# Kernel optimization log

Hardware: AMD Instinct MI355X
Metric: run time of the kernel (lower is better)

## Reference

```python
import jax, jax.numpy as jnp
import numpy as np

B, V, NV, NR, N, E, D, H, OUT, L = 4, 20, 8000, 200, 8000, 200000, 128, 128, 64, 3
DECAY = 0.03


def setup_inputs() -> dict:
    key = jax.random.key(0)
    ks = jax.random.split(key, 16)
    node_ids = jax.random.randint(ks[0], (N,), 0, NV)
    rel_ids = jax.random.randint(ks[1], (E,), 0, NR)
    edge_index = jax.random.randint(ks[2], (2, E), 0, N)
    batch = jnp.repeat(jnp.arange(B), N // B)  # sorted graph assignment, 2000 nodes/graph
    visit_node = (jax.random.uniform(ks[3], (B, V, NV)) < 0.3).astype(jnp.float32)
    ehr_nodes = (jax.random.uniform(ks[4], (B, NV)) < 0.1).astype(jnp.float32)
    s = lambda k, shape: jax.random.normal(k, shape, jnp.float32) * 0.05
    return dict(
        node_ids=node_ids, rel_ids=rel_ids, edge_index=edge_index, batch=batch,
        visit_node=visit_node, ehr_nodes=ehr_nodes,
        node_emb_w=s(ks[5], (NV, D)), rel_emb_w=s(ks[6], (NR, D)),
        lin_w=s(ks[7], (D, H)), lin_b=jnp.zeros((H,), jnp.float32),
        alpha_w=s(ks[8], (L, H)), alpha_b=jnp.zeros((L,), jnp.float32),
        beta_w=s(ks[9], (L, NV)), beta_b=jnp.zeros((L,), jnp.float32),
        conv_w=s(ks[10], (L, H, H)), conv_b=jnp.zeros((L, H), jnp.float32),
        wr_w=s(ks[11], (L, H)), wr_b=jnp.zeros((L,), jnp.float32),
        mlp_w=s(ks[12], (2 * H, OUT)), mlp_b=jnp.zeros((OUT,), jnp.float32),
    )


def reference(node_ids, rel_ids, edge_index, batch, visit_node, ehr_nodes,
              node_emb_w, rel_emb_w, lin_w, lin_b, alpha_w, alpha_b,
              beta_w, beta_b, conv_w, conv_b, wr_w, wr_b, mlp_w, mlp_b):
    # shared input projection (torch: self.lin applied to node and edge embeddings)
    x = node_emb_w[node_ids] @ lin_w + lin_b          # [N,H]
    edge_attr = rel_emb_w[rel_ids] @ lin_w + lin_b    # [E,H]

    # pack per-graph node features into dense [B, NV, H] (x_new in torch, fixed across layers)
    counts = jax.ops.segment_sum(jnp.ones((N,), jnp.float32), batch, B)            # [B]
    starts = jnp.concatenate([jnp.zeros((1,), jnp.int32),
                              jnp.cumsum(counts.astype(jnp.int32))[:-1]])
    local = jnp.arange(N) - starts[batch]                                          # position within graph
    x_pad = jnp.zeros((B, NV, H), jnp.float32).at[batch, local].set(x)

    lam = jnp.exp(DECAY * (V - jnp.arange(V, dtype=jnp.float32)))[None, :, None]   # [1,V,1]
    src, dst = edge_index[0], edge_index[1]
    eb, en = batch[src], node_ids[src]

    for l in range(L):
        # alpha attention over visits (softmax on visit axis)
        feat = visit_node[..., None] * x_pad[:, None]                              # [B,V,NV,H]
        alpha = jax.nn.softmax(jnp.einsum('bvnh,h->bvn', feat, alpha_w[l]) + alpha_b[l], axis=1)
        # beta: time-decayed visit attention
        beta = jnp.tanh(visit_node @ beta_w[l] + beta_b[l])[:, :, None] * lam      # [B,V,1]
        attn_full = alpha * beta                                                   # [B,V,NV]
        attn_e = attn_full[eb, 0, en][:, None]                                     # [E,1] (visit idx 0 as in source)
        # BiAttentionGNNConv: gather-mul-relu-scatter with edge attention
        w_rel = (edge_attr @ wr_w[l] + wr_b[l])[:, None]                           # [E,1]
        msg = jax.nn.relu(x[src] * attn_e + w_rel * edge_attr)                     # [E,H]
        agg = jax.ops.segment_sum(msg, dst, N)                                     # scatter-add to targets
        x = jax.nn.relu((agg + x) @ conv_w[l] + conv_b[l])                         # eps=0 -> (1+eps)*x = x; dropout=eval

    # joint patient representation
    x_graph = jax.ops.segment_sum(x, batch, B) / counts[:, None]                   # global mean pool
    x_node = (ehr_nodes @ node_emb_w) / jnp.sum(ehr_nodes, axis=1, keepdims=True)  # [B,D]
    x_node = x_node @ lin_w + lin_b
    logits = jnp.concatenate([x_graph, x_node], axis=1) @ mlp_w + mlp_b            # [B,OUT]
    return logits
```

## Files before the change

kernel.cpp:

```cpp
#include <hip/hip_runtime.h>

#define NN  8000
#define EE  200000
#define BB  4
#define VV  20
#define NVV 8000
#define NRR 200
#define HH  128
#define OO  64
#define LL  3
#define NPB 8

__global__ void k_zero(float* fz, int nf, int* iz, int ni) {
  int i = blockIdx.x * 256 + threadIdx.x;
  if (i < nf) fz[i] = 0.f;
  if (i < ni) iz[i] = 0;
}

__global__ __launch_bounds__(128) void k_proj_nodes(
    const int* __restrict__ node_ids, const float* __restrict__ emb,
    const float* __restrict__ lin_w, const float* __restrict__ lin_b,
    const float* __restrict__ alpha_w, float* __restrict__ x,
    float* __restrict__ snode)
{
  int blk = blockIdx.x, t = threadIdx.x;
  __shared__ float er[NPB][HH];
  __shared__ float part[LL][NPB][2];
  int base = blk * NPB;
  #pragma unroll
  for (int n = 0; n < NPB; ++n)
    er[n][t] = emb[node_ids[base + n] * HH + t];
  __syncthreads();
  float bt = lin_b[t];
  float acc[NPB];
  #pragma unroll
  for (int n = 0; n < NPB; ++n) acc[n] = bt;
  for (int d4 = 0; d4 < HH / 4; ++d4) {
    float e4[NPB][4];
    #pragma unroll
    for (int n = 0; n < NPB; ++n) {
      float4 v = *(const float4*)&er[n][d4 * 4];
      e4[n][0] = v.x; e4[n][1] = v.y; e4[n][2] = v.z; e4[n][3] = v.w;
    }
    #pragma unroll
    for (int j = 0; j < 4; ++j) {
      float lwv = lin_w[(d4 * 4 + j) * HH + t];
      #pragma unroll
      for (int n = 0; n < NPB; ++n) acc[n] += e4[n][j] * lwv;
    }
  }
  #pragma unroll
  for (int n = 0; n < NPB; ++n) x[(base + n) * HH + t] = acc[n];
  #pragma unroll
  for (int l = 0; l < LL; ++l) {
    float aw = alpha_w[l * HH + t];
    #pragma unroll
    for (int n = 0; n < NPB; ++n) {
      float v = acc[n] * aw;
      for (int off = 32; off > 0; off >>= 1) v += __shfl_down(v, off, 64);
      if ((t & 63) == 0) part[l][n][t >> 6] = v;
    }
  }
  __syncthreads();
  if (t < LL * NPB) {
    int l = t / NPB, n = t % NPB;
    snode[l * NN + base + n] = part[l][n][0] + part[l][n][1];
  }
}

__global__ __launch_bounds__(128) void k_proj_rels(
    const float* __restrict__ rel_emb, const float* __restrict__ lin_w,
    const float* __restrict__ lin_b, const float* __restrict__ wr_w,
    const float* __restrict__ wr_b, float* __restrict__ wrelp)
{
  int r = blockIdx.x, t = threadIdx.x;
  __shared__ float row[HH];
  __shared__ float part[LL][2];
  row[t] = rel_emb[r * HH + t];
  __syncthreads();
  float acc = lin_b[t];
  #pragma unroll 4
  for (int d = 0; d < HH; ++d) acc += row[d] * lin_w[d * HH + t];
  #pragma unroll
  for (int l = 0; l < LL; ++l) {
    float v = acc * wr_w[l * HH + t];
    for (int off = 32; off > 0; off >>= 1) v += __shfl_down(v, off, 64);
    if ((t & 63) == 0) part[l][t >> 6] = v;
  }
  __syncthreads();
  #pragma unroll
  for (int l = 0; l < LL; ++l) {
    float rd = part[l][0] + part[l][1] + wr_b[l];
    wrelp[(l * NRR + r) * HH + t] = rd * acc;
  }
}

__global__ __launch_bounds__(256) void k_beta(
    const float* __restrict__ visit_node, const float* __restrict__ beta_w,
    const float* __restrict__ beta_b, float* __restrict__ beta0)
{
  int l = blockIdx.x >> 2, b = blockIdx.x & 3, t = threadIdx.x;
  __shared__ float red[256];
  float acc = 0.f;
  for (int n = t; n < NVV; n += 256)
    acc += visit_node[(b * VV + 0) * NVV + n] * beta_w[l * NVV + n];
  red[t] = acc;
  __syncthreads();
  for (int s = 128; s > 0; s >>= 1) {
    if (t < s) red[t] += red[t + s];
    __syncthreads();
  }
  if (t == 0) beta0[l * BB + b] = tanhf(red[0] + beta_b[l]) * expf(0.03f * 20.0f);
}

__global__ __launch_bounds__(256) void k_attn(
    const float* __restrict__ visit_node, const float* __restrict__ snode,
    const float* __restrict__ alpha_b, float* __restrict__ attn0)
{
  int idx = blockIdx.x * 256 + threadIdx.x;
  if (idx >= BB * NVV) return;
  int b = idx / NVV, n = idx % NVV;
  float vn[VV];
  #pragma unroll
  for (int v = 0; v < VV; ++v) vn[v] = visit_node[(b * VV + v) * NVV + n];
  for (int l = 0; l < LL; ++l) {
    float s = (n < NN / BB) ? snode[l * NN + b * (NN / BB) + n] : 0.0f;
    float ab = alpha_b[l];
    float m = -1e30f;
    #pragma unroll
    for (int v = 0; v < VV; ++v) m = fmaxf(m, vn[v] * s + ab);
    float sum = 0.f;
    #pragma unroll
    for (int v = 0; v < VV; ++v) sum += expf(vn[v] * s + ab - m);
    attn0[(l * BB + b) * NVV + n] = expf(vn[0] * s + ab - m) / sum;
  }
}

__global__ void k_anode(const int* __restrict__ node_ids, const int* __restrict__ batch,
                        const float* __restrict__ attn0, const float* __restrict__ beta0,
                        float* __restrict__ anode)
{
  int i = blockIdx.x * 256 + threadIdx.x;
  if (i >= NN) return;
  int b = batch[i], nid = node_ids[i];
  #pragma unroll
  for (int l = 0; l < LL; ++l)
    anode[l * NN + i] = attn0[(l * BB + b) * NVV + nid] * beta0[l * BB + b];
}

__global__ void k_hist(const int* __restrict__ edge_index, int* __restrict__ deg) {
  int e = blockIdx.x * 256 + threadIdx.x;
  if (e >= EE) return;
  atomicAdd(&deg[edge_index[EE + e]], 1);
}

__global__ __launch_bounds__(1024) void k_scan(const int* __restrict__ deg,
                                               int* __restrict__ row_ptr)
{
  int t = threadIdx.x;
  __shared__ int ps[1024];
  int local[8];
  int base = t * 8;
  int s = 0;
  #pragma unroll
  for (int j = 0; j < 8; ++j) {
    int idx = base + j;
    int v = (idx < NN) ? deg[idx] : 0;
    local[j] = s; s += v;
  }
  ps[t] = s;
  __syncthreads();
  for (int off = 1; off < 1024; off <<= 1) {
    int v = (t >= off) ? ps[t - off] : 0;
    __syncthreads();
    ps[t] += v;
    __syncthreads();
  }
  int excl = (t == 0) ? 0 : ps[t - 1];
  #pragma unroll
  for (int j = 0; j < 8; ++j) {
    int idx = base + j;
    if (idx < NN) row_ptr[idx] = excl + local[j];
  }
  if (t == 1023) row_ptr[NN] = ps[1023];
}

__global__ void k_scatter(const int* __restrict__ edge_index, const int* __restrict__ rel_ids,
                          const int* __restrict__ row_ptr, int* __restrict__ cursor,
                          int2* __restrict__ csr_sr, float* __restrict__ csr_a,
                          const float* __restrict__ anode)
{
  int e = blockIdx.x * 256 + threadIdx.x;
  if (e >= EE) return;
  int src = edge_index[e];
  int dst = edge_index[EE + e];
  int rid = rel_ids[e];
  int p = row_ptr[dst] + atomicAdd(&cursor[dst], 1);
  csr_sr[p] = make_int2(src, rid);
  csr_a[0 * EE + p] = anode[0 * NN + src];
  csr_a[1 * EE + p] = anode[1 * NN + src];
  csr_a[2 * EE + p] = anode[2 * NN + src];
}

__global__ __launch_bounds__(256) void k_gather_conv(
    const int* __restrict__ row_ptr, const int2* __restrict__ csr_sr,
    const float* __restrict__ csr_a, const float* __restrict__ xin,
    const float* __restrict__ wrelp, const float* __restrict__ conv_w,
    const float* __restrict__ conv_b, float* __restrict__ xout, int l)
{
  int t = threadIdx.x;
  int sub = t >> 5, lane = t & 31;
  int i = blockIdx.x * NPB + sub;
  __shared__ float aggrow[NPB][HH];
  const float4* __restrict__ xin4 = (const float4*)xin;
  const float4* __restrict__ wr4 = (const float4*)wrelp + (size_t)l * NRR * 32;
  const float4* __restrict__ cw4 = (const float4*)conv_w + (size_t)l * HH * 32;
  const float* __restrict__ ca = csr_a + (size_t)l * EE;

  float4 acc = xin4[i * 32 + lane];
  int k0 = row_ptr[i], k1 = row_ptr[i + 1];
  int k = k0;
  for (; k + 1 < k1; k += 2) {
    int2 sr0 = csr_sr[k];
    int2 sr1 = csr_sr[k + 1];
    float a0 = ca[k], a1 = ca[k + 1];
    float4 x0 = xin4[sr0.x * 32 + lane];
    float4 w0 = wr4[sr0.y * 32 + lane];
    float4 x1 = xin4[sr1.x * 32 + lane];
    float4 w1 = wr4[sr1.y * 32 + lane];
    acc.x += fmaxf(x0.x * a0 + w0.x, 0.f) + fmaxf(x1.x * a1 + w1.x, 0.f);
    acc.y += fmaxf(x0.y * a0 + w0.y, 0.f) + fmaxf(x1.y * a1 + w1.y, 0.f);
    acc.z += fmaxf(x0.z * a0 + w0.z, 0.f) + fmaxf(x1.z * a1 + w1.z, 0.f);
    acc.w += fmaxf(x0.w * a0 + w0.w, 0.f) + fmaxf(x1.w * a1 + w1.w, 0.f);
  }
  if (k < k1) {
    int2 sr0 = csr_sr[k];
    float a0 = ca[k];
    float4 x0 = xin4[sr0.x * 32 + lane];
    float4 w0 = wr4[sr0.y * 32 + lane];
    acc.x += fmaxf(x0.x * a0 + w0.x, 0.f);
    acc.y += fmaxf(x0.y * a0 + w0.y, 0.f);
    acc.z += fmaxf(x0.z * a0 + w0.z, 0.f);
    acc.w += fmaxf(x0.w * a0 + w0.w, 0.f);
  }
  *(float4*)&aggrow[sub][lane * 4] = acc;
  __syncthreads();

  float4 o = ((const float4*)conv_b)[l * 32 + lane];
  for (int d4 = 0; d4 < HH / 4; ++d4) {
    float4 ag = *(const float4*)&aggrow[sub][d4 * 4];
    float4 c0 = cw4[(d4 * 4 + 0) * 32 + lane];
    float4 c1 = cw4[(d4 * 4 + 1) * 32 + lane];
    float4 c2 = cw4[(d4 * 4 + 2) * 32 + lane];
    float4 c3 = cw4[(d4 * 4 + 3) * 32 + lane];
    o.x += ag.x * c0.x + ag.y * c1.x + ag.z * c2.x + ag.w * c3.x;
    o.y += ag.x * c0.y + ag.y * c1.y + ag.z * c2.y + ag.w * c3.y;
    o.z += ag.x * c0.z + ag.y * c1.z + ag.z * c2.z + ag.w * c3.z;
    o.w += ag.x * c0.w + ag.y * c1.w + ag.z * c2.w + ag.w * c3.w;
  }
  o.x = fmaxf(o.x, 0.f); o.y = fmaxf(o.y, 0.f);
  o.z = fmaxf(o.z, 0.f); o.w = fmaxf(o.w, 0.f);
  ((float4*)xout)[i * 32 + lane] = o;
}

__global__ __launch_bounds__(128) void k_xgraph(
    const float* __restrict__ x, float* __restrict__ xg_raw)
{
  int b = blockIdx.x >> 4, c = blockIdx.x & 15, t = threadIdx.x;
  const int per = (NN / BB) / 16;
  int base = b * (NN / BB) + c * per;
  float acc = 0.f;
  for (int i = 0; i < per; ++i) acc += x[(base + i) * HH + t];
  atomicAdd(&xg_raw[b * HH + t], acc);
}

__global__ __launch_bounds__(128) void k_xnode(
    const float* __restrict__ ehr, const float* __restrict__ emb,
    float* __restrict__ xn_raw, float* __restrict__ denom)
{
  int b = blockIdx.x >> 5, c = blockIdx.x & 31, t = threadIdx.x;
  const int per = NVV / 32;
  int base = c * per;
  float acc = 0.f;
  for (int n = base; n < base + per; ++n)
    acc += ehr[b * NVV + n] * emb[n * HH + t];
  atomicAdd(&xn_raw[b * HH + t], acc);
  __shared__ float red[128];
  float dsum = 0.f;
  for (int n = base + t; n < base + per; n += 128) dsum += ehr[b * NVV + n];
  red[t] = dsum;
  __syncthreads();
  for (int s = 64; s > 0; s >>= 1) {
    if (t < s) red[t] += red[t + s];
    __syncthreads();
  }
  if (t == 0) atomicAdd(&denom[b], red[0]);
}

__global__ __launch_bounds__(128) void k_final(
    const float* __restrict__ xg_raw, const float* __restrict__ xn_raw,
    const float* __restrict__ denom, const float* __restrict__ lin_w,
    const float* __restrict__ lin_b, const float* __restrict__ mlp_w,
    const float* __restrict__ mlp_b, float* __restrict__ out)
{
  int b = blockIdx.x, t = threadIdx.x;
  __shared__ float xg[HH], xn[HH], xnp[HH];
  xg[t] = xg_raw[b * HH + t] * (1.0f / (NN / BB));
  xn[t] = xn_raw[b * HH + t] / denom[b];
  __syncthreads();
  float a3 = lin_b[t];
  #pragma unroll 4
  for (int d = 0; d < HH; ++d) a3 += xn[d] * lin_w[d * HH + t];
  xnp[t] = a3;
  __syncthreads();
  if (t < OO) {
    float a4 = mlp_b[t];
    #pragma unroll 4
    for (int h = 0; h < HH; ++h)
      a4 += xg[h] * mlp_w[h * OO + t] + xnp[h] * mlp_w[(HH + h) * OO + t];
    out[b * OO + t] = a4;
  }
}

extern "C" void kernel_launch(void* const* d_in, const int* in_sizes, int n_in,
                              void* d_out, int out_size, void* d_ws, size_t ws_size,
                              hipStream_t stream) {
  const int*   node_ids   = (const int*)d_in[0];
  const int*   rel_ids    = (const int*)d_in[1];
  const int*   edge_index = (const int*)d_in[2];
  const int*   batch      = (const int*)d_in[3];
  const float* visit_node = (const float*)d_in[4];
  const float* ehr        = (const float*)d_in[5];
  const float* node_emb   = (const float*)d_in[6];
  const float* rel_emb    = (const float*)d_in[7];
  const float* lin_w      = (const float*)d_in[8];
  const float* lin_b      = (const float*)d_in[9];
  const float* alpha_w    = (const float*)d_in[10];
  const float* alpha_b    = (const float*)d_in[11];
  const float* beta_w     = (const float*)d_in[12];
  const float* beta_b     = (const float*)d_in[13];
  const float* conv_w     = (const float*)d_in[14];
  const float* conv_b     = (const float*)d_in[15];
  const float* wr_w       = (const float*)d_in[16];
  const float* wr_b       = (const float*)d_in[17];
  const float* mlp_w      = (const float*)d_in[18];
  const float* mlp_b      = (const float*)d_in[19];
  float* out = (float*)d_out;

  float* ws = (float*)d_ws;
  float* xA     = ws; ws += NN * HH;
  float* xB     = ws; ws += NN * HH;
  float* wrelp  = ws; ws += LL * NRR * HH;
  float* snode  = ws; ws += LL * NN;
  float* beta0  = ws; ws += LL * BB;
  float* attn0  = ws; ws += LL * BB * NVV;
  float* anode  = ws; ws += LL * NN;
  float* xg_raw = ws; ws += BB * HH;
  float* xn_raw = ws; ws += BB * HH;
  float* denom  = ws; ws += BB;
  int* iws      = (int*)ws;
  int* deg      = iws; iws += NN;
  int* cursor   = iws; iws += NN;
  int* row_ptr  = iws; iws += NN + 2;
  int2* csr_sr  = (int2*)iws; iws += 2 * EE;
  float* csr_a  = (float*)iws;

  int nf = BB * HH * 2 + BB;
  int ni = 2 * NN;
  hipLaunchKernelGGL(k_zero, dim3((ni + 255) / 256), dim3(256), 0, stream,
                     xg_raw, nf, deg, ni);

  hipLaunchKernelGGL(k_proj_nodes, dim3(NN / NPB), dim3(HH), 0, stream,
                     node_ids, node_emb, lin_w, lin_b, alpha_w, xA, snode);
  hipLaunchKernelGGL(k_proj_rels, dim3(NRR), dim3(HH), 0, stream,
                     rel_emb, lin_w, lin_b, wr_w, wr_b, wrelp);
  hipLaunchKernelGGL(k_beta, dim3(LL * BB), dim3(256), 0, stream,
                     visit_node, beta_w, beta_b, beta0);
  hipLaunchKernelGGL(k_attn, dim3((BB * NVV + 255) / 256), dim3(256), 0, stream,
                     visit_node, snode, alpha_b, attn0);
  hipLaunchKernelGGL(k_anode, dim3((NN + 255) / 256), dim3(256), 0, stream,
                     node_ids, batch, attn0, beta0, anode);

  hipLaunchKernelGGL(k_hist, dim3((EE + 255) / 256), dim3(256), 0, stream,
                     edge_index, deg);
  hipLaunchKernelGGL(k_scan, dim3(1), dim3(1024), 0, stream, deg, row_ptr);
  hipLaunchKernelGGL(k_scatter, dim3((EE + 255) / 256), dim3(256), 0, stream,
                     edge_index, rel_ids, row_ptr, cursor, csr_sr, csr_a, anode);

  const float* xin = xA;
  float* xout = xB;
  for (int l = 0; l < LL; ++l) {
    hipLaunchKernelGGL(k_gather_conv, dim3(NN / NPB), dim3(256), 0, stream,
                       row_ptr, csr_sr, csr_a, xin, wrelp, conv_w, conv_b, xout, l);
    const float* tmp = xin; xin = xout; xout = (float*)tmp;
  }

  hipLaunchKernelGGL(k_xgraph, dim3(BB * 16), dim3(HH), 0, stream, xB, xg_raw);
  hipLaunchKernelGGL(k_xnode, dim3(BB * 32), dim3(HH), 0, stream,
                     ehr, node_emb, xn_raw, denom);
  hipLaunchKernelGGL(k_final, dim3(BB), dim3(HH), 0, stream,
                     xg_raw, xn_raw, denom, lin_w, lin_b, mlp_w, mlp_b, out);
}
```

Measured before the change: 320.7 us.

## Fuse small setup kernels and gather per-node attention directly in conv

Merges the zeroing, relation projection and beta reduction into one kernel. Attention is computed only for the nodes actually used, fused with the degree histogram. The two pooling kernels become one. The scatter no longer writes per-edge attention arrays; the gather kernel reads anode[src] directly and is unrolled by 4. This cuts launch count, the full attn0 table computation and per-edge attention writes, at the cost of an extra indirect load per edge in each conv layer.

```diff
diff --git a/kernel.cpp b/kernel.cpp
--- a/kernel.cpp
+++ b/kernel.cpp
@@ -10,12 +10,7 @@
 #define OO  64
 #define LL  3
 #define NPB 8
-
-__global__ void k_zero(float* fz, int nf, int* iz, int ni) {
-  int i = blockIdx.x * 256 + threadIdx.x;
-  if (i < nf) fz[i] = 0.f;
-  if (i < ni) iz[i] = 0;
-}
+#define NG  2000
 
 __global__ __launch_bounds__(128) void k_proj_nodes(
     const int* __restrict__ node_ids, const float* __restrict__ emb,
@@ -68,63 +63,70 @@
   }
 }
 
-__global__ __launch_bounds__(128) void k_proj_rels(
+__global__ __launch_bounds__(128) void k_prb(
     const float* __restrict__ rel_emb, const float* __restrict__ lin_w,
     const float* __restrict__ lin_b, const float* __restrict__ wr_w,
-    const float* __restrict__ wr_b, float* __restrict__ wrelp)
-{
-  int r = blockIdx.x, t = threadIdx.x;
-  __shared__ float row[HH];
-  __shared__ float part[LL][2];
-  row[t] = rel_emb[r * HH + t];
-  __syncthreads();
-  float acc = lin_b[t];
-  #pragma unroll 4
-  for (int d = 0; d < HH; ++d) acc += row[d] * lin_w[d * HH + t];
+    const float* __restrict__ wr_b, const float* __restrict__ visit_node,
+    const float* __restrict__ beta_w, const float* __restrict__ beta_b,
+    float* __restrict__ wrelp, float* __restrict__ beta0,
+    int* __restrict__ iz, float* __restrict__ fz)
+{
+  int blk = blockIdx.x, t = threadIdx.x;
+  int idx = blk * 128 + t;
+  if (idx < 2 * NN) iz[idx] = 0;
+  if (idx < BB * HH * 2 + BB) fz[idx] = 0.f;
+  if (blk < NRR) {
+    __shared__ float row[HH];
+    __shared__ float part[LL][2];
+    row[t] = rel_emb[blk * HH + t];
+    __syncthreads();
+    float acc = lin_b[t];
+    #pragma unroll 4
+    for (int d = 0; d < HH; ++d) acc += row[d] * lin_w[d * HH + t];
+    #pragma unroll
+    for (int l = 0; l < LL; ++l) {
+      float v = acc * wr_w[l * HH + t];
+      for (int off = 32; off > 0; off >>= 1) v += __shfl_down(v, off, 64);
+      if ((t & 63) == 0) part[l][t >> 6] = v;
+    }
+    __syncthreads();
+    #pragma unroll
+    for (int l = 0; l < LL; ++l) {
+      float rd = part[l][0] + part[l][1] + wr_b[l];
+      wrelp[(l * NRR + blk) * HH + t] = rd * acc;
+    }
+  } else {
+    int j = blk - NRR;
+    int l = j >> 2, b = j & 3;
+    float acc = 0.f;
+    for (int n = t; n < NVV; n += 128)
+      acc += visit_node[(b * VV + 0) * NVV + n] * beta_w[l * NVV + n];
+    for (int off = 32; off > 0; off >>= 1) acc += __shfl_down(acc, off, 64);
+    __shared__ float bred[2];
+    if ((t & 63) == 0) bred[t >> 6] = acc;
+    __syncthreads();
+    if (t == 0)
+      beta0[l * BB + b] = tanhf(bred[0] + bred[1] + beta_b[l]) * expf(0.03f * 20.0f);
+  }
+}
+
+__global__ __launch_bounds__(256) void k_anode_hist(
+    const int* __restrict__ node_ids, const int* __restrict__ batch,
+    const int* __restrict__ edge_index, const float* __restrict__ visit_node,
+    const float* __restrict__ snode, const float* __restrict__ alpha_b,
+    const float* __restrict__ beta0, float* __restrict__ anode,
+    int* __restrict__ deg)
+{
+  int idx = blockIdx.x * 256 + threadIdx.x;
+  if (idx < EE) atomicAdd(&deg[edge_index[EE + idx]], 1);
+  if (idx >= NN) return;
+  int b = batch[idx], nid = node_ids[idx];
+  float vn[VV];
+  #pragma unroll
+  for (int v = 0; v < VV; ++v) vn[v] = visit_node[(b * VV + v) * NVV + nid];
   #pragma unroll
   for (int l = 0; l < LL; ++l) {
-    float v = acc * wr_w[l * HH + t];
-    for (int off = 32; off > 0; off >>= 1) v += __shfl_down(v, off, 64);
-    if ((t & 63) == 0) part[l][t >> 6] = v;
-  }
-  __syncthreads();
-  #pragma unroll
-  for (int l = 0; l < LL; ++l) {
-    float rd = part[l][0] + part[l][1] + wr_b[l];
-    wrelp[(l * NRR + r) * HH + t] = rd * acc;
-  }
-}
-
-__global__ __launch_bounds__(256) void k_beta(
-    const float* __restrict__ visit_node, const float* __restrict__ beta_w,
-    const float* __restrict__ beta_b, float* __restrict__ beta0)
-{
-  int l = blockIdx.x >> 2, b = blockIdx.x & 3, t = threadIdx.x;
-  __shared__ float red[256];
-  float acc = 0.f;
-  for (int n = t; n < NVV; n += 256)
-    acc += visit_node[(b * VV + 0) * NVV + n] * beta_w[l * NVV + n];
-  red[t] = acc;
-  __syncthreads();
-  for (int s = 128; s > 0; s >>= 1) {
-    if (t < s) red[t] += red[t + s];
-    __syncthreads();
-  }
-  if (t == 0) beta0[l * BB + b] = tanhf(red[0] + beta_b[l]) * expf(0.03f * 20.0f);
-}
-
-__global__ __launch_bounds__(256) void k_attn(
-    const float* __restrict__ visit_node, const float* __restrict__ snode,
-    const float* __restrict__ alpha_b, float* __restrict__ attn0)
-{
-  int idx = blockIdx.x * 256 + threadIdx.x;
-  if (idx >= BB * NVV) return;
-  int b = idx / NVV, n = idx % NVV;
-  float vn[VV];
-  #pragma unroll
-  for (int v = 0; v < VV; ++v) vn[v] = visit_node[(b * VV + v) * NVV + n];
-  for (int l = 0; l < LL; ++l) {
-    float s = (n < NN / BB) ? snode[l * NN + b * (NN / BB) + n] : 0.0f;
+    float s = (nid < NG) ? snode[l * NN + b * NG + nid] : 0.0f;
     float ab = alpha_b[l];
     float m = -1e30f;
     #pragma unroll
@@ -132,26 +134,8 @@
     float sum = 0.f;
     #pragma unroll
     for (int v = 0; v < VV; ++v) sum += expf(vn[v] * s + ab - m);
-    attn0[(l * BB + b) * NVV + n] = expf(vn[0] * s + ab - m) / sum;
-  }
-}
-
-__global__ void k_anode(const int* __restrict__ node_ids, const int* __restrict__ batch,
-                        const float* __restrict__ attn0, const float* __restrict__ beta0,
-                        float* __restrict__ anode)
-{
-  int i = blockIdx.x * 256 + threadIdx.x;
-  if (i >= NN) return;
-  int b = batch[i], nid = node_ids[i];
-  #pragma unroll
-  for (int l = 0; l < LL; ++l)
-    anode[l * NN + i] = attn0[(l * BB + b) * NVV + nid] * beta0[l * BB + b];
-}
-
-__global__ void k_hist(const int* __restrict__ edge_index, int* __restrict__ deg) {
-  int e = blockIdx.x * 256 + threadIdx.x;
-  if (e >= EE) return;
-  atomicAdd(&deg[edge_index[EE + e]], 1);
+    anode[l * NN + idx] = (expf(vn[0] * s + ab - m) / sum) * beta0[l * BB + b];
+  }
 }
 
 __global__ __launch_bounds__(1024) void k_scan(const int* __restrict__ deg,
@@ -187,24 +171,18 @@
 
 __global__ void k_scatter(const int* __restrict__ edge_index, const int* __restrict__ rel_ids,
                           const int* __restrict__ row_ptr, int* __restrict__ cursor,
-                          int2* __restrict__ csr_sr, float* __restrict__ csr_a,
-                          const float* __restrict__ anode)
+                          int2* __restrict__ csr_sr)
 {
   int e = blockIdx.x * 256 + threadIdx.x;
   if (e >= EE) return;
-  int src = edge_index[e];
   int dst = edge_index[EE + e];
-  int rid = rel_ids[e];
   int p = row_ptr[dst] + atomicAdd(&cursor[dst], 1);
-  csr_sr[p] = make_int2(src, rid);
-  csr_a[0 * EE + p] = anode[0 * NN + src];
-  csr_a[1 * EE + p] = anode[1 * NN + src];
-  csr_a[2 * EE + p] = anode[2 * NN + src];
+  csr_sr[p] = make_int2(edge_index[e], rel_ids[e]);
 }
 
 __global__ __launch_bounds__(256) void k_gather_conv(
     const int* __restrict__ row_ptr, const int2* __restrict__ csr_sr,
-    const float* __restrict__ csr_a, const float* __restrict__ xin,
+    const float* __restrict__ anode, const float* __restrict__ xin,
     const float* __restrict__ wrelp, const float* __restrict__ conv_w,
     const float* __restrict__ conv_b, float* __restrict__ xout, int l)
 {
@@ -215,29 +193,32 @@
   const float4* __restrict__ xin4 = (const float4*)xin;
   const float4* __restrict__ wr4 = (const float4*)wrelp + (size_t)l * NRR * 32;
   const float4* __restrict__ cw4 = (const float4*)conv_w + (size_t)l * HH * 32;
-  const float* __restrict__ ca = csr_a + (size_t)l * EE;
+  const float* __restrict__ an = anode + (size_t)l * NN;
 
   float4 acc = xin4[i * 32 + lane];
   int k0 = row_ptr[i], k1 = row_ptr[i + 1];
   int k = k0;
-  for (; k + 1 < k1; k += 2) {
-    int2 sr0 = csr_sr[k];
-    int2 sr1 = csr_sr[k + 1];
-    float a0 = ca[k], a1 = ca[k + 1];
-    float4 x0 = xin4[sr0.x * 32 + lane];
-    float4 w0 = wr4[sr0.y * 32 + lane];
-    float4 x1 = xin4[sr1.x * 32 + lane];
-    float4 w1 = wr4[sr1.y * 32 + lane];
-    acc.x += fmaxf(x0.x * a0 + w0.x, 0.f) + fmaxf(x1.x * a1 + w1.x, 0.f);
-    acc.y += fmaxf(x0.y * a0 + w0.y, 0.f) + fmaxf(x1.y * a1 + w1.y, 0.f);
-    acc.z += fmaxf(x0.z * a0 + w0.z, 0.f) + fmaxf(x1.z * a1 + w1.z, 0.f);
-    acc.w += fmaxf(x0.w * a0 + w0.w, 0.f) + fmaxf(x1.w * a1 + w1.w, 0.f);
-  }
-  if (k < k1) {
-    int2 sr0 = csr_sr[k];
-    float a0 = ca[k];
-    float4 x0 = xin4[sr0.x * 32 + lane];
-    float4 w0 = wr4[sr0.y * 32 + lane];
+  for (; k + 3 < k1; k += 4) {
+    int2 s0 = csr_sr[k],     s1 = csr_sr[k + 1];
+    int2 s2 = csr_sr[k + 2], s3 = csr_sr[k + 3];
+    float a0 = an[s0.x], a1 = an[s1.x], a2 = an[s2.x], a3 = an[s3.x];
+    float4 x0 = xin4[s0.x * 32 + lane], w0 = wr4[s0.y * 32 + lane];
+    float4 x1 = xin4[s1.x * 32 + lane], w1 = wr4[s1.y * 32 + lane];
+    float4 x2 = xin4[s2.x * 32 + lane], w2 = wr4[s2.y * 32 + lane];
+    float4 x3 = xin4[s3.x * 32 + lane], w3 = wr4[s3.y * 32 + lane];
+    acc.x += fmaxf(x0.x * a0 + w0.x, 0.f) + fmaxf(x1.x * a1 + w1.x, 0.f)
+           + fmaxf(x2.x * a2 + w2.x, 0.f) + fmaxf(x3.x * a3 + w3.x, 0.f);
+    acc.y += fmaxf(x0.y * a0 + w0.y, 0.f) + fmaxf(x1.y * a1 + w1.y, 0.f)
+           + fmaxf(x2.y * a2 + w2.y, 0.f) + fmaxf(x3.y * a3 + w3.y, 0.f);
+    acc.z += fmaxf(x0.z * a0 + w0.z, 0.f) + fmaxf(x1.z * a1 + w1.z, 0.f)
+           + fmaxf(x2.z * a2 + w2.z, 0.f) + fmaxf(x3.z * a3 + w3.z, 0.f);
+    acc.w += fmaxf(x0.w * a0 + w0.w, 0.f) + fmaxf(x1.w * a1 + w1.w, 0.f)
+           + fmaxf(x2.w * a2 + w2.w, 0.f) + fmaxf(x3.w * a3 + w3.w, 0.f);
+  }
+  for (; k < k1; ++k) {
+    int2 s0 = csr_sr[k];
+    float a0 = an[s0.x];
+    float4 x0 = xin4[s0.x * 32 + lane], w0 = wr4[s0.y * 32 + lane];
     acc.x += fmaxf(x0.x * a0 + w0.x, 0.f);
     acc.y += fmaxf(x0.y * a0 + w0.y, 0.f);
     acc.z += fmaxf(x0.z * a0 + w0.z, 0.f);
@@ -263,38 +244,39 @@
   ((float4*)xout)[i * 32 + lane] = o;
 }
 
-__global__ __launch_bounds__(128) void k_xgraph(
-    const float* __restrict__ x, float* __restrict__ xg_raw)
-{
-  int b = blockIdx.x >> 4, c = blockIdx.x & 15, t = threadIdx.x;
-  const int per = (NN / BB) / 16;
-  int base = b * (NN / BB) + c * per;
-  float acc = 0.f;
-  for (int i = 0; i < per; ++i) acc += x[(base + i) * HH + t];
-  atomicAdd(&xg_raw[b * HH + t], acc);
-}
-
-__global__ __launch_bounds__(128) void k_xnode(
-    const float* __restrict__ ehr, const float* __restrict__ emb,
+__global__ __launch_bounds__(128) void k_pool(
+    const float* __restrict__ x, const float* __restrict__ ehr,
+    const float* __restrict__ emb, float* __restrict__ xg_raw,
     float* __restrict__ xn_raw, float* __restrict__ denom)
 {
-  int b = blockIdx.x >> 5, c = blockIdx.x & 31, t = threadIdx.x;
-  const int per = NVV / 32;
-  int base = c * per;
-  float acc = 0.f;
-  for (int n = base; n < base + per; ++n)
-    acc += ehr[b * NVV + n] * emb[n * HH + t];
-  atomicAdd(&xn_raw[b * HH + t], acc);
-  __shared__ float red[128];
-  float dsum = 0.f;
-  for (int n = base + t; n < base + per; n += 128) dsum += ehr[b * NVV + n];
-  red[t] = dsum;
-  __syncthreads();
-  for (int s = 64; s > 0; s >>= 1) {
-    if (t < s) red[t] += red[t + s];
-    __syncthreads();
-  }
-  if (t == 0) atomicAdd(&denom[b], red[0]);
+  int t = threadIdx.x;
+  if (blockIdx.x < 64) {
+    int b = blockIdx.x >> 4, c = blockIdx.x & 15;
+    const int per = NG / 16;
+    int base = b * NG + c * per;
+    float acc = 0.f;
+    for (int i = 0; i < per; ++i) acc += x[(base + i) * HH + t];
+    atomicAdd(&xg_raw[b * HH + t], acc);
+  } else {
+    int ib = blockIdx.x - 64;
+    int b = ib >> 5, c = ib & 31;
+    const int per = NVV / 32;
+    int base = c * per;
+    float acc = 0.f;
+    for (int n = base; n < base + per; ++n)
+      acc += ehr[b * NVV + n] * emb[n * HH + t];
+    atomicAdd(&xn_raw[b * HH + t], acc);
+    __shared__ float red[128];
+    float dsum = 0.f;
+    for (int n = base + t; n < base + per; n += 128) dsum += ehr[b * NVV + n];
+    red[t] = dsum;
+    __syncthreads();
+    for (int s = 64; s > 0; s >>= 1) {
+      if (t < s) red[t] += red[t + s];
+      __syncthreads();
+    }
+    if (t == 0) atomicAdd(&denom[b], red[0]);
+  }
 }
 
 __global__ __launch_bounds__(128) void k_final(
@@ -305,7 +287,7 @@
 {
   int b = blockIdx.x, t = threadIdx.x;
   __shared__ float xg[HH], xn[HH], xnp[HH];
-  xg[t] = xg_raw[b * HH + t] * (1.0f / (NN / BB));
+  xg[t] = xg_raw[b * HH + t] * (1.0f / NG);
   xn[t] = xn_raw[b * HH + t] / denom[b];
   __syncthreads();
   float a3 = lin_b[t];
@@ -353,7 +335,6 @@
   float* wrelp  = ws; ws += LL * NRR * HH;
   float* snode  = ws; ws += LL * NN;
   float* beta0  = ws; ws += LL * BB;
-  float* attn0  = ws; ws += LL * BB * NVV;
   float* anode  = ws; ws += LL * NN;
   float* xg_raw = ws; ws += BB * HH;
   float* xn_raw = ws; ws += BB * HH;
@@ -362,42 +343,28 @@
   int* deg      = iws; iws += NN;
   int* cursor   = iws; iws += NN;
   int* row_ptr  = iws; iws += NN + 2;
-  int2* csr_sr  = (int2*)iws; iws += 2 * EE;
-  float* csr_a  = (float*)iws;
-
-  int nf = BB * HH * 2 + BB;
-  int ni = 2 * NN;
-  hipLaunchKernelGGL(k_zero, dim3((ni + 255) / 256), dim3(256), 0, stream,
-                     xg_raw, nf, deg, ni);
+  int2* csr_sr  = (int2*)iws;
 
   hipLaunchKernelGGL(k_proj_nodes, dim3(NN / NPB), dim3(HH), 0, stream,
                      node_ids, node_emb, lin_w, lin_b, alpha_w, xA, snode);
-  hipLaunchKernelGGL(k_proj_rels, dim3(NRR), dim3(HH), 0, stream,
-                     rel_emb, lin_w, lin_b, wr_w, wr_b, wrelp);
-  hipLaunchKernelGGL(k_beta, dim3(LL * BB), dim3(256), 0, stream,
-                     visit_node, beta_w, beta_b, beta0);
-  hipLaunchKernelGGL(k_attn, dim3((BB * NVV + 255) / 256), dim3(256), 0, stream,
-                     visit_node, snode, alpha_b, attn0);
-  hipLaunchKernelGGL(k_anode, dim3((NN + 255) / 256), dim3(256), 0, stream,
-                     node_ids, batch, attn0, beta0, anode);
-
-  hipLaunchKernelGGL(k_hist, dim3((EE + 255) / 256), dim3(256), 0, stream,
-                     edge_index, deg);
+  hipLaunchKernelGGL(k_prb, dim3(NRR + LL * BB), dim3(HH), 0, stream,
+                     rel_emb, lin_w, lin_b, wr_w, wr_b, visit_node, beta_w,
+                     beta_b, wrelp, beta0, deg, xg_raw);
+  hipLaunchKernelGGL(k_anode_hist, dim3((EE + 255) / 256), dim3(256), 0, stream,
+                     node_ids, batch, edge_index, visit_node, snode, alpha_b,
+                     beta0, anode, deg);
   hipLaunchKernelGGL(k_scan, dim3(1), dim3(1024), 0, stream, deg, row_ptr);
   hipLaunchKernelGGL(k_scatter, dim3((EE + 255) / 256), dim3(256), 0, stream,
-                     edge_index, rel_ids, row_ptr, cursor, csr_sr, csr_a, anode);
-
+                     edge_index, rel_ids, row_ptr, cursor, csr_sr);
   const float* xin = xA;
   float* xout = xB;
   for (int l = 0; l < LL; ++l) {
     hipLaunchKernelGGL(k_gather_conv, dim3(NN / NPB), dim3(256), 0, stream,
-                       row_ptr, csr_sr, csr_a, xin, wrelp, conv_w, conv_b, xout, l);
+                       row_ptr, csr_sr, anode, xin, wrelp, conv_w, conv_b, xout, l);
     const float* tmp = xin; xin = xout; xout = (float*)tmp;
   }
-
-  hipLaunchKernelGGL(k_xgraph, dim3(BB * 16), dim3(HH), 0, stream, xB, xg_raw);
-  hipLaunchKernelGGL(k_xnode, dim3(BB * 32), dim3(HH), 0, stream,
-                     ehr, node_emb, xn_raw, denom);
+  hipLaunchKernelGGL(k_pool, dim3(64 + 128), dim3(HH), 0, stream,
+                     xB, ehr, node_emb, xg_raw, xn_raw, denom);
   hipLaunchKernelGGL(k_final, dim3(BB), dim3(HH), 0, stream,
                      xg_raw, xn_raw, denom, lin_w, lin_b, mlp_w, mlp_b, out);
 }
```

Result: faster. 311.3 us (-2.9%).
